# Optimization experiments

Measured on AMD Instinct MI355X. Metric: run time of the kernel, lower is better.

Reference implementation:

```python
import jax, jax.numpy as jnp
import numpy as np

B, IN_SIZE, P = 16384, 4096, 8
D = IN_SIZE // P  # 512


def setup_inputs() -> dict:
    key = jax.random.key(0)
    ks = jax.random.split(key, 10)
    bound = 1.0 / np.sqrt(D)  # fan_in = int_dim
    return {
        "x": jax.random.normal(ks[0], (B, IN_SIZE), dtype=jnp.float32),
        "weights1": jax.random.uniform(ks[1], (P, D, D), jnp.float32, -bound, bound),
        "bias1": jax.random.uniform(ks[2], (IN_SIZE,), jnp.float32, -bound, bound),
        "weights2": jax.random.uniform(ks[3], (P, D, D), jnp.float32, -bound, bound),
        "bias2": jax.random.uniform(ks[4], (IN_SIZE,), jnp.float32, -bound, bound),
        # trainable swish params (init 0 as in torch code)
        "gamma1": jnp.zeros((IN_SIZE,), jnp.float32),
        "beta1": jnp.zeros((IN_SIZE,), jnp.float32),
        "gamma3": jnp.zeros((IN_SIZE,), jnp.float32),
        "beta3": jnp.zeros((IN_SIZE,), jnp.float32),
        # Affine norms (scalar gain/bias)
        "gain1": jnp.ones((1,), jnp.float32),
        "nbias1": jnp.zeros((1,), jnp.float32),
        "gain3": jnp.ones((1,), jnp.float32),
        "nbias3": jnp.zeros((1,), jnp.float32),
    }


def _swish(x, gamma, beta):
    # f(x) = (gamma + sigmoid(beta*x) * (1-gamma)) * x
    return (gamma + jax.nn.sigmoid(beta * x) * (1.0 - gamma)) * x


def _block_matmul(x, w):
    # x: [B, IN_SIZE] -> [B, P, D]; block-diagonal matmul == batched per-partition GEMM
    xb = x.reshape(x.shape[0], P, D)
    return jnp.einsum("bpd,pde->bpe", xb, w).reshape(x.shape[0], IN_SIZE)


def reference(x, weights1, bias1, weights2, bias2, gamma1, beta1, gamma3, beta3,
              gain1, nbias1, gain3, nbias3):
    o1 = _swish(_block_matmul(x * gain1 + nbias1, weights1) + bias1, gamma1, beta1)
    o2 = _swish(_block_matmul(o1 * gain3 + nbias3, weights2) + bias2, gamma3, beta3) + x
    return o2
```

## Files before the change

### kernel.cpp

```cpp
#include <hip/hip_runtime.h>
#include <cstdint>
#include <cstddef>


#define B_ROWS 16384
#define IN_SZ  4096
#define P_PART 8
#define D_DIM  512
#define M_BLK  64

typedef unsigned short ushort_t;
typedef __attribute__((ext_vector_type(8))) short short8;
typedef __attribute__((ext_vector_type(4))) float f32x4;

__device__ inline unsigned short f2bf(float f) {
  union { float f; unsigned int u; } c; c.f = f;
  unsigned int u = c.u;
  return (unsigned short)((u + 0x7fffu + ((u >> 16) & 1u)) >> 16);
}

__device__ inline int swz(int m, int c) { return m * D_DIM + (c ^ ((m & 7) << 3)); }

__global__ __launch_bounds__(256) void wconv_kernel(const float* __restrict__ w1,
                                                    const float* __restrict__ w2,
                                                    ushort_t* __restrict__ wt1,
                                                    ushort_t* __restrict__ wt2) {
  __shared__ float tile[64][68];
  const int p = blockIdx.z & 7;
  const float*  src = (blockIdx.z < 8) ? w1 : w2;
  ushort_t*     dst = (blockIdx.z < 8) ? wt1 : wt2;
  const int k0 = blockIdx.x * 64;
  const int n0 = blockIdx.y * 64;
  const int t = threadIdx.x;

  const float* base = src + ((size_t)p * D_DIM + k0) * D_DIM + n0;
#pragma unroll
  for (int i = 0; i < 4; ++i) {
    int f = t + i * 256;
    int kr = f >> 4;
    int c4 = f & 15;
    float4 v = *(const float4*)(base + (size_t)kr * D_DIM + c4 * 4);
    *(float4*)(&tile[kr][c4 * 4]) = v;
  }
  __syncthreads();
  ushort_t* obase = dst + ((size_t)p * D_DIM + n0) * D_DIM + k0;
#pragma unroll
  for (int i = 0; i < 4; ++i) {
    int f = t + i * 256;
    int nr = f >> 4;
    int kc = (f & 15) * 4;
    unsigned int lo = f2bf(tile[kc + 0][nr]) | ((unsigned int)f2bf(tile[kc + 1][nr]) << 16);
    unsigned int hi = f2bf(tile[kc + 2][nr]) | ((unsigned int)f2bf(tile[kc + 3][nr]) << 16);
    uint2 pk; pk.x = lo; pk.y = hi;
    *(uint2*)(obase + (size_t)nr * D_DIM + kc) = pk;
  }
}

__global__ __launch_bounds__(1024, 4) void fused_kernel(
    const float* __restrict__ x,
    const ushort_t* __restrict__ wt1, const ushort_t* __restrict__ wt2,
    const float* __restrict__ bias1, const float* __restrict__ gamma1,
    const float* __restrict__ beta1,
    const float* __restrict__ bias2, const float* __restrict__ gamma3,
    const float* __restrict__ beta3,
    const float* __restrict__ gain1, const float* __restrict__ nbias1,
    const float* __restrict__ gain3, const float* __restrict__ nbias3,
    float* __restrict__ out) {
  __shared__ __align__(16) ushort_t Xs[M_BLK * D_DIM];

  const int t = threadIdx.x;
  const int lane = t & 63, wid = t >> 6;
  const int l15 = lane & 15, quad = lane >> 4;
  const int p  = blockIdx.x;
  const int m0 = blockIdx.y * M_BLK;

  const float g1 = gain1[0], nb1 = nbias1[0];
  const float g3 = gain3[0], nb3 = nbias3[0];

  {
    const float* xb = x + (size_t)m0 * IN_SZ + (size_t)p * D_DIM;
#pragma unroll
    for (int i = 0; i < 8; ++i) {
      int g = t + i * 1024;
      int m = g >> 7;
      int c = (g & 127) * 4;
      float4 v = *(const float4*)(xb + (size_t)m * IN_SZ + c);
      uint2 pk;
      pk.x = f2bf(v.x * g1 + nb1) | ((unsigned int)f2bf(v.y * g1 + nb1) << 16);
      pk.y = f2bf(v.z * g1 + nb1) | ((unsigned int)f2bf(v.w * g1 + nb1) << 16);
      *(uint2*)(&Xs[swz(m, c)]) = pk;
    }
  }
  __syncthreads();

  f32x4 acc[2][4];
#pragma unroll
  for (int i = 0; i < 2; ++i)
#pragma unroll
    for (int j = 0; j < 4; ++j) acc[i][j] = (f32x4)(0.0f);

  {
    const ushort_t* w1b = wt1 + (size_t)p * D_DIM * D_DIM
                              + (size_t)(wid * 32 + l15) * D_DIM;
    short8 aw[3][2];
#define LDW1(bi, s) do { const int kof_ = (s) * 32 + quad * 8;                     \
      aw[bi][0] = *(const short8*)(w1b + kof_);                                    \
      aw[bi][1] = *(const short8*)(w1b + (size_t)16 * D_DIM + kof_); } while (0)
    LDW1(0, 0);
    LDW1(1, 1);
#pragma unroll
    for (int s = 0; s < 16; ++s) {
      if (s + 2 < 16) LDW1((s + 2) % 3, s + 2);
      const int kof = s * 32 + quad * 8;
      short8 b[4];
#pragma unroll
      for (int j = 0; j < 4; ++j)
        b[j] = *(const short8*)(&Xs[swz(j * 16 + l15, kof)]);
#pragma unroll
      for (int i = 0; i < 2; ++i)
#pragma unroll
        for (int j = 0; j < 4; ++j)
          acc[i][j] = __builtin_amdgcn_mfma_f32_16x16x32_bf16(aw[s % 3][i], b[j], acc[i][j], 0, 0, 0);
    }
#undef LDW1
  }

  __syncthreads();

#pragma unroll
  for (int i = 0; i < 2; ++i) {
    const int n = wid * 32 + i * 16 + quad * 4;
    const int col = p * D_DIM + n;
    const float4 bv = *(const float4*)(bias1 + col);
    const float4 ga = *(const float4*)(gamma1 + col);
    const float4 be = *(const float4*)(beta1 + col);
#pragma unroll
    for (int j = 0; j < 4; ++j) {
      const int m = j * 16 + l15;
      float o[4];
#pragma unroll
      for (int r = 0; r < 4; ++r) {
        float v = acc[i][j][r] + ((const float*)&bv)[r];
        float g = ((const float*)&ga)[r];
        float sg = 1.0f / (1.0f + __expf(-((const float*)&be)[r] * v));
        o[r] = ((g + sg * (1.0f - g)) * v) * g3 + nb3;
      }
      uint2 pk;
      pk.x = f2bf(o[0]) | ((unsigned int)f2bf(o[1]) << 16);
      pk.y = f2bf(o[2]) | ((unsigned int)f2bf(o[3]) << 16);
      *(uint2*)(&Xs[swz(m, n)]) = pk;
    }
  }
  __syncthreads();

  f32x4 acc2[4][2];
#pragma unroll
  for (int i = 0; i < 4; ++i)
#pragma unroll
    for (int j = 0; j < 2; ++j) acc2[i][j] = (f32x4)(0.0f);

  {
    const ushort_t* w2b = wt2 + (size_t)p * D_DIM * D_DIM
                              + (size_t)(wid * 32 + l15) * D_DIM;
    short8 bw[3][2];
#define LDW2(bi, s) do { const int kof_ = (s) * 32 + quad * 8;                     \
      bw[bi][0] = *(const short8*)(w2b + kof_);                                    \
      bw[bi][1] = *(const short8*)(w2b + (size_t)16 * D_DIM + kof_); } while (0)
    LDW2(0, 0);
    LDW2(1, 1);
#pragma unroll
    for (int s = 0; s < 16; ++s) {
      if (s + 2 < 16) LDW2((s + 2) % 3, s + 2);
      const int kof = s * 32 + quad * 8;
      short8 a[4];
#pragma unroll
      for (int i = 0; i < 4; ++i)
        a[i] = *(const short8*)(&Xs[swz(i * 16 + l15, kof)]);
#pragma unroll
      for (int i = 0; i < 4; ++i)
#pragma unroll
        for (int j = 0; j < 2; ++j)
          acc2[i][j] = __builtin_amdgcn_mfma_f32_16x16x32_bf16(a[i], bw[s % 3][j], acc2[i][j], 0, 0, 0);
    }
#undef LDW2
  }

  const int colg0 = p * D_DIM + wid * 32;
#pragma unroll
  for (int j = 0; j < 2; ++j) {
    const int col = colg0 + j * 16 + l15;
    const float bv = bias2[col], ga = gamma3[col], be = beta3[col];
#pragma unroll
    for (int i = 0; i < 4; ++i) {
      const int r0 = m0 + i * 16 + quad * 4;
#pragma unroll
      for (int r = 0; r < 4; ++r) {
        float v = acc2[i][j][r] + bv;
        float sg = 1.0f / (1.0f + __expf(-be * v));
        float o = (ga + sg * (1.0f - ga)) * v;
        const size_t idx = (size_t)(r0 + r) * IN_SZ + col;
        out[idx] = o + x[idx];
      }
    }
  }
}

extern "C" void kernel_launch(void* const* d_in, const int* in_sizes, int n_in,
                              void* d_out, int out_size, void* d_ws, size_t ws_size,
                              hipStream_t stream) {
  const float* x      = (const float*)d_in[0];
  const float* w1     = (const float*)d_in[1];
  const float* b1     = (const float*)d_in[2];
  const float* w2     = (const float*)d_in[3];
  const float* b2     = (const float*)d_in[4];
  const float* gamma1 = (const float*)d_in[5];
  const float* beta1  = (const float*)d_in[6];
  const float* gamma3 = (const float*)d_in[7];
  const float* beta3  = (const float*)d_in[8];
  const float* gain1  = (const float*)d_in[9];
  const float* nbias1 = (const float*)d_in[10];
  const float* gain3  = (const float*)d_in[11];
  const float* nbias3 = (const float*)d_in[12];
  float* out = (float*)d_out;

  ushort_t* wt1 = (ushort_t*)d_ws;
  ushort_t* wt2 = wt1 + (size_t)P_PART * D_DIM * D_DIM;

  wconv_kernel<<<dim3(8, 8, 16), 256, 0, stream>>>(w1, w2, wt1, wt2);
  fused_kernel<<<dim3(P_PART, B_ROWS / M_BLK), 1024, 0, stream>>>(
      x, wt1, wt2, b1, gamma1, beta1, b2, gamma3, beta3,
      gain1, nbias1, gain3, nbias3, out);
}
```

Before: 758.0 us.

## Make fused blocks persistent over four row tiles with register-prefetched x

Each block now handles four consecutive 64-row tiles instead of one, so the grid shrinks by four. The next tile's x slice is loaded into registers while the current tile's two GEMMs run, and it is converted to bf16 in shared memory at the end of the iteration. The triple-buffered weight register prefetch is dropped in favour of direct per-step loads. This cuts block launch and prologue cost and overlaps x loads with compute, but it adds register pressure (32 extra floats per thread), an extra barrier per tile, and fewer blocks to balance across CUs.

```diff
diff --git a/kernel.cpp b/kernel.cpp
--- a/kernel.cpp
+++ b/kernel.cpp
@@ -8,6 +8,7 @@
 #define P_PART 8
 #define D_DIM  512
 #define M_BLK  64
+#define T_TILES 4
 
 typedef unsigned short ushort_t;
 typedef __attribute__((ext_vector_type(8))) short short8;
@@ -72,134 +73,149 @@
   const int lane = t & 63, wid = t >> 6;
   const int l15 = lane & 15, quad = lane >> 4;
   const int p  = blockIdx.x;
-  const int m0 = blockIdx.y * M_BLK;
+  const int by = blockIdx.y;
 
   const float g1 = gain1[0], nb1 = nbias1[0];
   const float g3 = gain3[0], nb3 = nbias3[0];
 
+  const ushort_t* w1b = wt1 + (size_t)p * D_DIM * D_DIM + (size_t)(wid * 32 + l15) * D_DIM;
+  const ushort_t* w2b = wt2 + (size_t)p * D_DIM * D_DIM + (size_t)(wid * 32 + l15) * D_DIM;
+
+  float4 xf[8];
   {
-    const float* xb = x + (size_t)m0 * IN_SZ + (size_t)p * D_DIM;
+    const float* xb = x + (size_t)(by * T_TILES) * M_BLK * IN_SZ + (size_t)p * D_DIM;
 #pragma unroll
     for (int i = 0; i < 8; ++i) {
       int g = t + i * 1024;
-      int m = g >> 7;
-      int c = (g & 127) * 4;
-      float4 v = *(const float4*)(xb + (size_t)m * IN_SZ + c);
-      uint2 pk;
-      pk.x = f2bf(v.x * g1 + nb1) | ((unsigned int)f2bf(v.y * g1 + nb1) << 16);
-      pk.y = f2bf(v.z * g1 + nb1) | ((unsigned int)f2bf(v.w * g1 + nb1) << 16);
-      *(uint2*)(&Xs[swz(m, c)]) = pk;
-    }
-  }
-  __syncthreads();
-
-  f32x4 acc[2][4];
-#pragma unroll
-  for (int i = 0; i < 2; ++i)
-#pragma unroll
-    for (int j = 0; j < 4; ++j) acc[i][j] = (f32x4)(0.0f);
-
-  {
-    const ushort_t* w1b = wt1 + (size_t)p * D_DIM * D_DIM
-                              + (size_t)(wid * 32 + l15) * D_DIM;
-    short8 aw[3][2];
-#define LDW1(bi, s) do { const int kof_ = (s) * 32 + quad * 8;                     \
-      aw[bi][0] = *(const short8*)(w1b + kof_);                                    \
-      aw[bi][1] = *(const short8*)(w1b + (size_t)16 * D_DIM + kof_); } while (0)
-    LDW1(0, 0);
-    LDW1(1, 1);
+      xf[i] = *(const float4*)(xb + (size_t)(g >> 7) * IN_SZ + (g & 127) * 4);
+    }
+  }
+#pragma unroll
+  for (int i = 0; i < 8; ++i) {
+    int g = t + i * 1024;
+    int m = g >> 7, c = (g & 127) * 4;
+    uint2 pk;
+    pk.x = f2bf(xf[i].x * g1 + nb1) | ((unsigned int)f2bf(xf[i].y * g1 + nb1) << 16);
+    pk.y = f2bf(xf[i].z * g1 + nb1) | ((unsigned int)f2bf(xf[i].w * g1 + nb1) << 16);
+    *(uint2*)(&Xs[swz(m, c)]) = pk;
+  }
+
+#pragma unroll 1
+  for (int tt = 0; tt < T_TILES; ++tt) {
+    const int m0 = (by * T_TILES + tt) * M_BLK;
+    __syncthreads();
+
+    if (tt + 1 < T_TILES) {
+      const float* xb = x + (size_t)(m0 + M_BLK) * IN_SZ + (size_t)p * D_DIM;
+#pragma unroll
+      for (int i = 0; i < 8; ++i) {
+        int g = t + i * 1024;
+        xf[i] = *(const float4*)(xb + (size_t)(g >> 7) * IN_SZ + (g & 127) * 4);
+      }
+    }
+
+    f32x4 acc[2][4];
+#pragma unroll
+    for (int i = 0; i < 2; ++i)
+#pragma unroll
+      for (int j = 0; j < 4; ++j) acc[i][j] = (f32x4)(0.0f);
+
 #pragma unroll
     for (int s = 0; s < 16; ++s) {
-      if (s + 2 < 16) LDW1((s + 2) % 3, s + 2);
       const int kof = s * 32 + quad * 8;
+      short8 a0 = *(const short8*)(w1b + kof);
+      short8 a1 = *(const short8*)(w1b + (size_t)16 * D_DIM + kof);
       short8 b[4];
 #pragma unroll
       for (int j = 0; j < 4; ++j)
         b[j] = *(const short8*)(&Xs[swz(j * 16 + l15, kof)]);
 #pragma unroll
-      for (int i = 0; i < 2; ++i)
-#pragma unroll
-        for (int j = 0; j < 4; ++j)
-          acc[i][j] = __builtin_amdgcn_mfma_f32_16x16x32_bf16(aw[s % 3][i], b[j], acc[i][j], 0, 0, 0);
-    }
-#undef LDW1
-  }
-
-  __syncthreads();
-
-#pragma unroll
-  for (int i = 0; i < 2; ++i) {
-    const int n = wid * 32 + i * 16 + quad * 4;
-    const int col = p * D_DIM + n;
-    const float4 bv = *(const float4*)(bias1 + col);
-    const float4 ga = *(const float4*)(gamma1 + col);
-    const float4 be = *(const float4*)(beta1 + col);
-#pragma unroll
-    for (int j = 0; j < 4; ++j) {
-      const int m = j * 16 + l15;
-      float o[4];
-#pragma unroll
-      for (int r = 0; r < 4; ++r) {
-        float v = acc[i][j][r] + ((const float*)&bv)[r];
-        float g = ((const float*)&ga)[r];
-        float sg = 1.0f / (1.0f + __expf(-((const float*)&be)[r] * v));
-        o[r] = ((g + sg * (1.0f - g)) * v) * g3 + nb3;
-      }
-      uint2 pk;
-      pk.x = f2bf(o[0]) | ((unsigned int)f2bf(o[1]) << 16);
-      pk.y = f2bf(o[2]) | ((unsigned int)f2bf(o[3]) << 16);
-      *(uint2*)(&Xs[swz(m, n)]) = pk;
-    }
-  }
-  __syncthreads();
-
-  f32x4 acc2[4][2];
-#pragma unroll
-  for (int i = 0; i < 4; ++i)
-#pragma unroll
-    for (int j = 0; j < 2; ++j) acc2[i][j] = (f32x4)(0.0f);
-
-  {
-    const ushort_t* w2b = wt2 + (size_t)p * D_DIM * D_DIM
-                              + (size_t)(wid * 32 + l15) * D_DIM;
-    short8 bw[3][2];
-#define LDW2(bi, s) do { const int kof_ = (s) * 32 + quad * 8;                     \
-      bw[bi][0] = *(const short8*)(w2b + kof_);                                    \
-      bw[bi][1] = *(const short8*)(w2b + (size_t)16 * D_DIM + kof_); } while (0)
-    LDW2(0, 0);
-    LDW2(1, 1);
+      for (int j = 0; j < 4; ++j) {
+        acc[0][j] = __builtin_amdgcn_mfma_f32_16x16x32_bf16(a0, b[j], acc[0][j], 0, 0, 0);
+        acc[1][j] = __builtin_amdgcn_mfma_f32_16x16x32_bf16(a1, b[j], acc[1][j], 0, 0, 0);
+      }
+    }
+
+    __syncthreads();
+
+#pragma unroll
+    for (int i = 0; i < 2; ++i) {
+      const int n = wid * 32 + i * 16 + quad * 4;
+      const int col = p * D_DIM + n;
+      const float4 bv = *(const float4*)(bias1 + col);
+      const float4 ga = *(const float4*)(gamma1 + col);
+      const float4 be = *(const float4*)(beta1 + col);
+#pragma unroll
+      for (int j = 0; j < 4; ++j) {
+        const int m = j * 16 + l15;
+        float o[4];
+#pragma unroll
+        for (int r = 0; r < 4; ++r) {
+          float v = acc[i][j][r] + ((const float*)&bv)[r];
+          float g = ((const float*)&ga)[r];
+          float sg = 1.0f / (1.0f + __expf(-((const float*)&be)[r] * v));
+          o[r] = ((g + sg * (1.0f - g)) * v) * g3 + nb3;
+        }
+        uint2 pk;
+        pk.x = f2bf(o[0]) | ((unsigned int)f2bf(o[1]) << 16);
+        pk.y = f2bf(o[2]) | ((unsigned int)f2bf(o[3]) << 16);
+        *(uint2*)(&Xs[swz(m, n)]) = pk;
+      }
+    }
+    __syncthreads();
+
+    f32x4 acc2[4][2];
+#pragma unroll
+    for (int i = 0; i < 4; ++i)
+#pragma unroll
+      for (int j = 0; j < 2; ++j) acc2[i][j] = (f32x4)(0.0f);
+
 #pragma unroll
     for (int s = 0; s < 16; ++s) {
-      if (s + 2 < 16) LDW2((s + 2) % 3, s + 2);
       const int kof = s * 32 + quad * 8;
+      short8 b0 = *(const short8*)(w2b + kof);
+      short8 b1 = *(const short8*)(w2b + (size_t)16 * D_DIM + kof);
       short8 a[4];
 #pragma unroll
       for (int i = 0; i < 4; ++i)
         a[i] = *(const short8*)(&Xs[swz(i * 16 + l15, kof)]);
 #pragma unroll
-      for (int i = 0; i < 4; ++i)
-#pragma unroll
-        for (int j = 0; j < 2; ++j)
-          acc2[i][j] = __builtin_amdgcn_mfma_f32_16x16x32_bf16(a[i], bw[s % 3][j], acc2[i][j], 0, 0, 0);
-    }
-#undef LDW2
-  }
-
-  const int colg0 = p * D_DIM + wid * 32;
-#pragma unroll
-  for (int j = 0; j < 2; ++j) {
-    const int col = colg0 + j * 16 + l15;
-    const float bv = bias2[col], ga = gamma3[col], be = beta3[col];
-#pragma unroll
-    for (int i = 0; i < 4; ++i) {
-      const int r0 = m0 + i * 16 + quad * 4;
-#pragma unroll
-      for (int r = 0; r < 4; ++r) {
-        float v = acc2[i][j][r] + bv;
-        float sg = 1.0f / (1.0f + __expf(-be * v));
-        float o = (ga + sg * (1.0f - ga)) * v;
-        const size_t idx = (size_t)(r0 + r) * IN_SZ + col;
-        out[idx] = o + x[idx];
+      for (int i = 0; i < 4; ++i) {
+        acc2[i][0] = __builtin_amdgcn_mfma_f32_16x16x32_bf16(a[i], b0, acc2[i][0], 0, 0, 0);
+        acc2[i][1] = __builtin_amdgcn_mfma_f32_16x16x32_bf16(a[i], b1, acc2[i][1], 0, 0, 0);
+      }
+    }
+
+    __syncthreads();
+
+    const int colg0 = p * D_DIM + wid * 32;
+#pragma unroll
+    for (int j = 0; j < 2; ++j) {
+      const int col = colg0 + j * 16 + l15;
+      const float bv = bias2[col], ga = gamma3[col], be = beta3[col];
+#pragma unroll
+      for (int i = 0; i < 4; ++i) {
+        const int r0 = m0 + i * 16 + quad * 4;
+#pragma unroll
+        for (int r = 0; r < 4; ++r) {
+          float v = acc2[i][j][r] + bv;
+          float sg = 1.0f / (1.0f + __expf(-be * v));
+          float o = (ga + sg * (1.0f - ga)) * v;
+          const size_t idx = (size_t)(r0 + r) * IN_SZ + col;
+          out[idx] = o + x[idx];
+        }
+      }
+    }
+
+    if (tt + 1 < T_TILES) {
+#pragma unroll
+      for (int i = 0; i < 8; ++i) {
+        int g = t + i * 1024;
+        int m = g >> 7, c = (g & 127) * 4;
+        uint2 pk;
+        pk.x = f2bf(xf[i].x * g1 + nb1) | ((unsigned int)f2bf(xf[i].y * g1 + nb1) << 16);
+        pk.y = f2bf(xf[i].z * g1 + nb1) | ((unsigned int)f2bf(xf[i].w * g1 + nb1) << 16);
+        *(uint2*)(&Xs[swz(m, c)]) = pk;
       }
     }
   }
@@ -227,7 +243,7 @@
   ushort_t* wt2 = wt1 + (size_t)P_PART * D_DIM * D_DIM;
 
   wconv_kernel<<<dim3(8, 8, 16), 256, 0, stream>>>(w1, w2, wt1, wt2);
-  fused_kernel<<<dim3(P_PART, B_ROWS / M_BLK), 1024, 0, stream>>>(
+  fused_kernel<<<dim3(P_PART, B_ROWS / (M_BLK * T_TILES)), 1024, 0, stream>>>(
       x, wt1, wt2, b1, gamma1, beta1, b2, gamma3, beta3,
       gain1, nbias1, gain3, nbias3, out);
 }
```

Result: slower. 1.698 ms (+124.0%).
